# Optimization experiments

Hardware: AMD Instinct MI355X
Metric: run time of the kernel (lower is better)

Reference implementation:

```python
import jax, jax.numpy as jnp
import numpy as np

N_NODES = 50000
N_EDGES = 800000
IN_CH = 128
OUT_CH = 32
HEADS = 4
NEG_SLOPE = 0.2


def setup_inputs() -> dict:
    key = jax.random.key(0)
    k = jax.random.split(key, 6)
    x = jax.random.normal(k[0], (N_NODES, IN_CH), dtype=jnp.float32)
    edge_index = jax.random.randint(k[1], (2, N_EDGES), 0, N_NODES, dtype=jnp.int32)
    # Glorot-style init for the learned parameters of GATConv
    W = jax.random.normal(k[2], (IN_CH, HEADS * OUT_CH), dtype=jnp.float32) / np.sqrt(IN_CH)
    att_src = jax.random.normal(k[3], (HEADS, OUT_CH), dtype=jnp.float32) / np.sqrt(OUT_CH)
    att_dst = jax.random.normal(k[4], (HEADS, OUT_CH), dtype=jnp.float32) / np.sqrt(OUT_CH)
    bias = jnp.zeros((HEADS * OUT_CH,), dtype=jnp.float32)
    return {"x": x, "edge_index": edge_index, "W": W,
            "att_src": att_src, "att_dst": att_dst, "bias": bias}


def reference(x, edge_index, W, att_src, att_dst, bias):
    # PyG GATConv, single layer: concat=True, add_self_loops=True, neg_slope=0.2
    N = x.shape[0]
    H, C = att_src.shape
    # add self loops (PyG default)
    loop = jnp.arange(N, dtype=edge_index.dtype)
    src = jnp.concatenate([edge_index[0], loop])  # [E+N] message sources j
    dst = jnp.concatenate([edge_index[1], loop])  # [E+N] message targets i
    # linear projection per head
    h = (x @ W).reshape(N, H, C)                  # [N,H,C]
    a_src = jnp.einsum('nhc,hc->nh', h, att_src)  # [N,H]
    a_dst = jnp.einsum('nhc,hc->nh', h, att_dst)  # [N,H]
    # edge-wise attention logits with LeakyReLU
    e = jax.nn.leaky_relu(a_src[src] + a_dst[dst], NEG_SLOPE)  # [E',H]
    # segment softmax over incoming edges of each destination node
    m = jax.ops.segment_max(e, dst, num_segments=N)            # [N,H]
    expe = jnp.exp(e - m[dst])
    denom = jax.ops.segment_sum(expe, dst, num_segments=N)     # [N,H]
    alpha = expe / denom[dst]                                  # [E',H]
    # scatter-aggregate weighted messages
    out = jax.ops.segment_sum(h[src] * alpha[:, :, None], dst, num_segments=N)  # [N,H,C]
    return out.reshape(N, H * C) + bias
```

## Files before the change

### kernel.cpp

```cpp
#include <hip/hip_runtime.h>


constexpr int N_NODES = 50000;
constexpr int N_EDGES = 800000;
constexpr int HC      = 128;
constexpr float NEG_SLOPE = 0.2f;
constexpr int M_TILES = N_NODES / 16;
constexpr int NB_PASSA = 256;
constexpr int NB_GEMM  = 512;
constexpr int EPB      = N_EDGES / NB_PASSA;
constexpr int BIN      = 64;
constexpr int NBKT     = 256;
constexpr int BWK      = 196;
constexpr int CAP      = 36;
constexpr int LDA      = 136;

typedef short short8 __attribute__((ext_vector_type(8)));
typedef float f32x4  __attribute__((ext_vector_type(4)));

__device__ inline unsigned short f2bf(float f) {
    unsigned int u = __float_as_uint(f);
    u += 0x7FFF + ((u >> 16) & 1);
    return (unsigned short)(u >> 16);
}


__global__ __launch_bounds__(256) void gemm_passA(
    const float* __restrict__ x,
    const float* __restrict__ W,
    const float* __restrict__ att_src, const float* __restrict__ att_dst,
    const int* __restrict__ esrc, const int* __restrict__ edst,
    unsigned short* __restrict__ hb,
    float* __restrict__ a_src, float* __restrict__ a_dst,
    unsigned int* __restrict__ seg,
    int* __restrict__ seg_cnt)
{
    __shared__ int cnt_l[NBKT];
    __shared__ unsigned short As[2][16][LDA];
    if (blockIdx.x < NB_PASSA) {
        const int p = blockIdx.x;
        cnt_l[threadIdx.x] = 0;
        __syncthreads();
        const int e0 = p * EPB, e1 = e0 + EPB;
        for (int e = e0 + threadIdx.x; e < e1; e += 256) {
            const int d = edst[e];
            const int s = esrc[e];
            const int b = d / BWK;
            const int pos = atomicAdd(&cnt_l[b], 1);
            if (pos < CAP)
                seg[((p * NBKT) + b) * CAP + pos] =
                    ((unsigned int)s << 8) | (unsigned int)(d - b * BWK);
        }
        __syncthreads();
        seg_cnt[p * NBKT + threadIdx.x] = min(cnt_l[threadIdx.x], CAP);
        return;
    }
    const int tid  = threadIdx.x;
    const int wave = tid >> 6;
    const int lane = tid & 63;
    const int n0   = (wave & 1) * 64;
    const int l15  = lane & 15;
    const int quad = lane >> 4;

    short8 bfrag[4][4];
    #pragma unroll
    for (int t = 0; t < 4; ++t)
        #pragma unroll
        for (int ks = 0; ks < 4; ++ks) {
            short8 b;
            #pragma unroll
            for (int j = 0; j < 8; ++j)
                b[j] = (short)f2bf(W[(ks * 32 + quad * 8 + j) * 128 + n0 + t * 16 + l15]);
            bfrag[t][ks] = b;
        }

    float asw[4], adw[4];
    #pragma unroll
    for (int t = 0; t < 4; ++t) {
        asw[t] = att_src[n0 + t * 16 + l15];
        adw[t] = att_dst[n0 + t * 16 + l15];
    }

    const int gb = blockIdx.x - NB_PASSA;
    for (int mtb = gb * 2; mtb < M_TILES; mtb += NB_GEMM * 2) {
        #pragma unroll
        for (int j = 0; j < 4; ++j) {
            const int g   = tid + j * 256;
            const int tl  = g >> 9;
            const int w   = g & 511;
            const int row = w >> 5;
            const int c4  = w & 31;
            const int mts = mtb + tl;
            if (mts < M_TILES) {
                const float4 u = *(const float4*)&x[(size_t)(mts * 16 + row) * 128 + c4 * 4];
                ushort4 v;
                v.x = f2bf(u.x); v.y = f2bf(u.y); v.z = f2bf(u.z); v.w = f2bf(u.w);
                *(ushort4*)&As[tl][row][c4 * 4] = v;
            }
        }
        __syncthreads();

        const int mt = mtb + (wave >> 1);
        if (mt < M_TILES) {
            const int m0 = mt * 16;
            const int tl = wave >> 1;

            short8 afrag[4];
            #pragma unroll
            for (int ks = 0; ks < 4; ++ks)
                afrag[ks] = *(const short8*)&As[tl][l15][ks * 32 + quad * 8];

            f32x4 acc[4];
            #pragma unroll
            for (int t = 0; t < 4; ++t) acc[t] = (f32x4){0.f, 0.f, 0.f, 0.f};

            #pragma unroll
            for (int ks = 0; ks < 4; ++ks)
                #pragma unroll
                for (int t = 0; t < 4; ++t)
                    acc[t] = __builtin_amdgcn_mfma_f32_16x16x32_bf16(afrag[ks], bfrag[t][ks], acc[t], 0, 0, 0);

            #pragma unroll
            for (int t = 0; t < 4; ++t)
                #pragma unroll
                for (int r = 0; r < 4; ++r)
                    hb[(m0 + quad * 4 + r) * 128 + n0 + t * 16 + l15] = f2bf(acc[t][r]);

            float hs[2][4] = {{0.f,0.f,0.f,0.f},{0.f,0.f,0.f,0.f}};
            float hd[2][4] = {{0.f,0.f,0.f,0.f},{0.f,0.f,0.f,0.f}};
            #pragma unroll
            for (int t = 0; t < 4; ++t)
                #pragma unroll
                for (int r = 0; r < 4; ++r) {
                    hs[t >> 1][r] += acc[t][r] * asw[t];
                    hd[t >> 1][r] += acc[t][r] * adw[t];
                }
            #pragma unroll
            for (int off = 1; off < 16; off <<= 1)
                #pragma unroll
                for (int g = 0; g < 2; ++g)
                    #pragma unroll
                    for (int r = 0; r < 4; ++r) {
                        hs[g][r] += __shfl_xor(hs[g][r], off);
                        hd[g][r] += __shfl_xor(hd[g][r], off);
                    }
            if (l15 == 0) {
                const int hb0 = n0 >> 5;
                #pragma unroll
                for (int g = 0; g < 2; ++g)
                    #pragma unroll
                    for (int r = 0; r < 4; ++r) {
                        a_src[(m0 + quad * 4 + r) * 4 + hb0 + g] = hs[g][r];
                        a_dst[(m0 + quad * 4 + r) * 4 + hb0 + g] = hd[g][r];
                    }
            }
        }
        __syncthreads();
    }
}


__global__ __launch_bounds__(256) void passB(
    const unsigned int* __restrict__ seg, const int* __restrict__ seg_cnt,
    int* __restrict__ deg, unsigned short* __restrict__ csr_bin)
{
    __shared__ unsigned short bin_l[BWK * BIN];
    __shared__ int deg_l[BWK];
    const int b   = blockIdx.x;
    const int tid = threadIdx.x;
    const int nb  = min(BWK, N_NODES - b * BWK);

    for (int i = tid; i < BWK; i += 256) deg_l[i] = 0;
    __syncthreads();

    const int cnt = seg_cnt[tid * NBKT + b];
    const uint4* s4 = (const uint4*)&seg[((size_t)(tid * NBKT) + b) * CAP];
    for (int i = 0; i < cnt; i += 4) {
        const uint4 u = s4[i >> 2];
        const int rem = cnt - i;
        {
            const int pos = atomicAdd(&deg_l[u.x & 255u], 1);
            if (pos < BIN - 1) bin_l[(u.x & 255u) * BIN + 1 + pos] = (unsigned short)(u.x >> 8);
        }
        if (rem > 1) {
            const int pos = atomicAdd(&deg_l[u.y & 255u], 1);
            if (pos < BIN - 1) bin_l[(u.y & 255u) * BIN + 1 + pos] = (unsigned short)(u.y >> 8);
        }
        if (rem > 2) {
            const int pos = atomicAdd(&deg_l[u.z & 255u], 1);
            if (pos < BIN - 1) bin_l[(u.z & 255u) * BIN + 1 + pos] = (unsigned short)(u.z >> 8);
        }
        if (rem > 3) {
            const int pos = atomicAdd(&deg_l[u.w & 255u], 1);
            if (pos < BIN - 1) bin_l[(u.w & 255u) * BIN + 1 + pos] = (unsigned short)(u.w >> 8);
        }
    }
    __syncthreads();

    uint4* dst = (uint4*)(csr_bin + (size_t)b * BWK * BIN);
    const uint4* srcl = (const uint4*)bin_l;
    constexpr int NVEC = BWK * BIN / 8;
    for (int k = tid; k < NVEC; k += 256) dst[k] = srcl[k];
    for (int i = tid; i < nb; i += 256) deg[b * BWK + i] = deg_l[i];
}


__global__ __launch_bounds__(256) void gat_agg(
    const int* __restrict__ deg, const unsigned short* __restrict__ csr_bin,
    const unsigned short* __restrict__ hb, const float* __restrict__ a_src,
    const float* __restrict__ a_dst, const float* __restrict__ bias,
    float* __restrict__ out)
{
    __shared__ float ws[4][256];
    const int wv = threadIdx.x >> 6;
    const int node = blockIdx.x * 4 + wv;
    if (node >= N_NODES) return;
    const int lane = threadIdx.x & 63;
    const int q    = lane >> 4;
    const int li   = lane & 15;
    const int ch0  = li * 8;
    const int hd   = li >> 2;
    const float4 ad4 = *(const float4*)&a_dst[node * 4];
    int m = deg[node] + 1;
    if (m > BIN) m = BIN;

    int sv = 0;
    if (lane < m)
        sv = (lane == 0) ? node : (int)csr_bin[(size_t)node * BIN + lane];
    if (lane < m) {
        const float4 av = *(const float4*)&a_src[sv * 4];
        float t; float4 w4;
        t = av.x + ad4.x; t = t > 0.f ? t : NEG_SLOPE * t; w4.x = __expf(t);
        t = av.y + ad4.y; t = t > 0.f ? t : NEG_SLOPE * t; w4.y = __expf(t);
        t = av.z + ad4.z; t = t > 0.f ? t : NEG_SLOPE * t; w4.z = __expf(t);
        t = av.w + ad4.w; t = t > 0.f ? t : NEG_SLOPE * t; w4.w = __expf(t);
        *(float4*)&ws[wv][lane * 4] = w4;
    }

    float acc[8] = {0.f,0.f,0.f,0.f,0.f,0.f,0.f,0.f};
    float dsum = 0.f;

    const int i0 = (q < m) ? q : 0;
    uint4 hv0 = *(const uint4*)&hb[(size_t)__shfl(sv, i0) * 128 + ch0];
    const int e1 = 4 + q;
    const int i1 = (e1 < m) ? e1 : 0;
    uint4 hv1 = *(const uint4*)&hb[(size_t)__shfl(sv, i1) * 128 + ch0];

    for (int j = 0; j < m; j += 4) {
        const int en  = j + 8 + q;
        const int idn = en < m ? en : 0;
        const int s_n = __shfl(sv, idn);
        const uint4 hv2 = *(const uint4*)&hb[(size_t)s_n * 128 + ch0];

        const int ei  = j + q;
        const int idx = ei < m ? ei : j;
        float w = ws[wv][idx * 4 + hd];
        if (ei >= m) w = 0.f;
        acc[0] += w * __uint_as_float(hv0.x << 16);
        acc[1] += w * __uint_as_float(hv0.x & 0xFFFF0000u);
        acc[2] += w * __uint_as_float(hv0.y << 16);
        acc[3] += w * __uint_as_float(hv0.y & 0xFFFF0000u);
        acc[4] += w * __uint_as_float(hv0.z << 16);
        acc[5] += w * __uint_as_float(hv0.z & 0xFFFF0000u);
        acc[6] += w * __uint_as_float(hv0.w << 16);
        acc[7] += w * __uint_as_float(hv0.w & 0xFFFF0000u);
        dsum += w;
        hv0 = hv1; hv1 = hv2;
    }

    #pragma unroll
    for (int off = 16; off <= 32; off <<= 1) {
        #pragma unroll
        for (int r = 0; r < 8; ++r) acc[r] += __shfl_xor(acc[r], off);
        dsum += __shfl_xor(dsum, off);
    }
    if (q == 0) {
        const float inv = 1.f / dsum;
        const float4 b0 = *(const float4*)&bias[ch0];
        const float4 b1 = *(const float4*)&bias[ch0 + 4];
        float4 o0, o1;
        o0.x = acc[0]*inv + b0.x; o0.y = acc[1]*inv + b0.y;
        o0.z = acc[2]*inv + b0.z; o0.w = acc[3]*inv + b0.w;
        o1.x = acc[4]*inv + b1.x; o1.y = acc[5]*inv + b1.y;
        o1.z = acc[6]*inv + b1.z; o1.w = acc[7]*inv + b1.w;
        *(float4*)&out[(size_t)node * HC + ch0]     = o0;
        *(float4*)&out[(size_t)node * HC + ch0 + 4] = o1;
    }
}

extern "C" void kernel_launch(void* const* d_in, const int* in_sizes, int n_in,
                              void* d_out, int out_size, void* d_ws, size_t ws_size,
                              hipStream_t stream) {
    const float* x       = (const float*)d_in[0];
    const int*   ei      = (const int*)  d_in[1];
    const float* W       = (const float*)d_in[2];
    const float* att_src = (const float*)d_in[3];
    const float* att_dst = (const float*)d_in[4];
    const float* bias    = (const float*)d_in[5];
    float* out = (float*)d_out;

    char* p = (char*)d_ws;
    unsigned short* hb  = (unsigned short*)p; p += (size_t)N_NODES * HC * 2;
    float* a_src = (float*)p; p += (size_t)N_NODES * 4 * 4;
    float* a_dst = (float*)p; p += (size_t)N_NODES * 4 * 4;
    unsigned short* csr_bin = (unsigned short*)p; p += (size_t)NBKT * BWK * BIN * 2;
    int* deg     = (int*)p;   p += N_NODES * 4;
    unsigned int* seg = (unsigned int*)p; p += (size_t)NB_PASSA * NBKT * CAP * 4;
    int* seg_cnt = (int*)p;   p += NB_PASSA * NBKT * 4;

    const int* esrc = ei;
    const int* edst = ei + N_EDGES;

    gemm_passA<<<NB_PASSA + NB_GEMM, 256, 0, stream>>>(x, W, att_src, att_dst,
                                                       esrc, edst, hb, a_src, a_dst,
                                                       seg, seg_cnt);
    passB     <<<NBKT, 256, 0, stream>>>(seg, seg_cnt, deg, csr_bin);
    gat_agg   <<<(N_NODES + 3) / 4, 256, 0, stream>>>(deg, csr_bin, hb, a_src,
                                                      a_dst, bias, out);
}
```

Baseline: 145.9 us.

## Split aggregation into two channel-half launches with eight edges per step

```diff
diff --git a/kernel.cpp b/kernel.cpp
--- a/kernel.cpp
+++ b/kernel.cpp
@@ -205,6 +205,7 @@
 }
 
 
+template<int CH0>
 __global__ __launch_bounds__(256) void gat_agg(
     const int* __restrict__ deg, const unsigned short* __restrict__ csr_bin,
     const unsigned short* __restrict__ hb, const float* __restrict__ a_src,
@@ -216,10 +217,10 @@
     const int node = blockIdx.x * 4 + wv;
     if (node >= N_NODES) return;
     const int lane = threadIdx.x & 63;
-    const int q    = lane >> 4;
-    const int li   = lane & 15;
-    const int ch0  = li * 8;
-    const int hd   = li >> 2;
+    const int e8   = lane >> 3;
+    const int c8   = lane & 7;
+    const int ch0  = CH0 + c8 * 8;
+    const int hd   = ch0 >> 5;
     const float4 ad4 = *(const float4*)&a_dst[node * 4];
     int m = deg[node] + 1;
     if (m > BIN) m = BIN;
@@ -240,41 +241,36 @@
     float acc[8] = {0.f,0.f,0.f,0.f,0.f,0.f,0.f,0.f};
     float dsum = 0.f;
 
-    const int i0 = (q < m) ? q : 0;
-    uint4 hv0 = *(const uint4*)&hb[(size_t)__shfl(sv, i0) * 128 + ch0];
-    const int e1 = 4 + q;
-    const int i1 = (e1 < m) ? e1 : 0;
-    uint4 hv1 = *(const uint4*)&hb[(size_t)__shfl(sv, i1) * 128 + ch0];
-
-    for (int j = 0; j < m; j += 4) {
-        const int en  = j + 8 + q;
-        const int idn = en < m ? en : 0;
-        const int s_n = __shfl(sv, idn);
-        const uint4 hv2 = *(const uint4*)&hb[(size_t)s_n * 128 + ch0];
-
-        const int ei  = j + q;
+    const int i0 = (e8 < m) ? e8 : 0;
+    uint4 hv = *(const uint4*)&hb[(size_t)__shfl(sv, i0) * 128 + ch0];
+    for (int j = 0; j < m; j += 8) {
+        const int ei  = j + e8;
         const int idx = ei < m ? ei : j;
+        const int ein = ei + 8;
+        const int idxn = ein < m ? ein : 0;
+        const int s_nxt = __shfl(sv, idxn);
+        const uint4 hvn = *(const uint4*)&hb[(size_t)s_nxt * 128 + ch0];
         float w = ws[wv][idx * 4 + hd];
         if (ei >= m) w = 0.f;
-        acc[0] += w * __uint_as_float(hv0.x << 16);
-        acc[1] += w * __uint_as_float(hv0.x & 0xFFFF0000u);
-        acc[2] += w * __uint_as_float(hv0.y << 16);
-        acc[3] += w * __uint_as_float(hv0.y & 0xFFFF0000u);
-        acc[4] += w * __uint_as_float(hv0.z << 16);
-        acc[5] += w * __uint_as_float(hv0.z & 0xFFFF0000u);
-        acc[6] += w * __uint_as_float(hv0.w << 16);
-        acc[7] += w * __uint_as_float(hv0.w & 0xFFFF0000u);
+        acc[0] += w * __uint_as_float(hv.x << 16);
+        acc[1] += w * __uint_as_float(hv.x & 0xFFFF0000u);
+        acc[2] += w * __uint_as_float(hv.y << 16);
+        acc[3] += w * __uint_as_float(hv.y & 0xFFFF0000u);
+        acc[4] += w * __uint_as_float(hv.z << 16);
+        acc[5] += w * __uint_as_float(hv.z & 0xFFFF0000u);
+        acc[6] += w * __uint_as_float(hv.w << 16);
+        acc[7] += w * __uint_as_float(hv.w & 0xFFFF0000u);
         dsum += w;
-        hv0 = hv1; hv1 = hv2;
+        hv = hvn;
     }
 
     #pragma unroll
-    for (int off = 16; off <= 32; off <<= 1) {
+    for (int off = 8; off <= 32; off <<= 1) {
         #pragma unroll
         for (int r = 0; r < 8; ++r) acc[r] += __shfl_xor(acc[r], off);
         dsum += __shfl_xor(dsum, off);
     }
-    if (q == 0) {
+    if (lane < 8) {
         const float inv = 1.f / dsum;
         const float4 b0 = *(const float4*)&bias[ch0];
         const float4 b1 = *(const float4*)&bias[ch0 + 4];
@@ -314,7 +310,9 @@
     gemm_passA<<<NB_PASSA + NB_GEMM, 256, 0, stream>>>(x, W, att_src, att_dst,
                                                        esrc, edst, hb, a_src, a_dst,
                                                        seg, seg_cnt);
-    passB     <<<NBKT, 256, 0, stream>>>(seg, seg_cnt, deg, csr_bin);
-    gat_agg   <<<(N_NODES + 3) / 4, 256, 0, stream>>>(deg, csr_bin, hb, a_src,
-                                                      a_dst, bias, out);
-}
+    passB      <<<NBKT, 256, 0, stream>>>(seg, seg_cnt, deg, csr_bin);
+    gat_agg<0> <<<(N_NODES + 3) / 4, 256, 0, stream>>>(deg, csr_bin, hb, a_src,
+                                                       a_dst, bias, out);
+    gat_agg<64><<<(N_NODES + 3) / 4, 256, 0, stream>>>(deg, csr_bin, hb, a_src,
+                                                       a_dst, bias, out);
+}
```

New measurement: 156.7 us. 7.4% more time.
